# Optimization experiments

Measured on AMD Instinct MI355X. Metric: run time of the kernel, lower is better.

The kernel has to match this reference:

```python
import jax, jax.numpy as jnp
import numpy as np

INPUT_DIMS = [300, 74, 35]
HIDDEN_DIMS = [512, 256, 256]
OUT_CELL = 256
OUT_DIM = 7
B, T = 128, 256


def setup_inputs() -> dict:
    key = jax.random.key(0)
    ks = jax.random.split(key, 32)
    inp = {}
    for i, d in enumerate(INPUT_DIMS):
        inp[f"x{i}"] = jax.random.normal(ks[i], (B, T, d), dtype=jnp.float32)
    ki = 3
    for i, (d, h) in enumerate(zip(INPUT_DIMS, HIDDEN_DIMS)):
        s_ih = 1.0 / np.sqrt(h)
        inp[f"W_ih{i}"] = jax.random.uniform(ks[ki + 0], (4 * h, d), jnp.float32, -s_ih, s_ih)
        inp[f"W_hh{i}"] = jax.random.uniform(ks[ki + 1], (4 * h, h), jnp.float32, -s_ih, s_ih)
        inp[f"b_ih{i}"] = jax.random.uniform(ks[ki + 2], (4 * h,), jnp.float32, -s_ih, s_ih)
        inp[f"b_hh{i}"] = jax.random.uniform(ks[ki + 3], (4 * h,), jnp.float32, -s_ih, s_ih)
        ki += 4
    H = sum(HIDDEN_DIMS)
    s1 = 1.0 / np.sqrt(H)
    s2 = 1.0 / np.sqrt(OUT_CELL)
    inp["fc_W1"] = jax.random.uniform(ks[ki + 0], (OUT_CELL, H), jnp.float32, -s1, s1)
    inp["fc_b1"] = jax.random.uniform(ks[ki + 1], (OUT_CELL,), jnp.float32, -s1, s1)
    inp["fc_W2"] = jax.random.uniform(ks[ki + 2], (OUT_DIM, OUT_CELL), jnp.float32, -s2, s2)
    inp["fc_b2"] = jax.random.uniform(ks[ki + 3], (OUT_DIM,), jnp.float32, -s2, s2)
    return inp


def _run_lstm(x, W_ih, W_hh, b_ih, b_hh):
    # x: [B, T, d] -> hidden trajectory [B, T, h]; PyTorch LSTMCell gate order i,f,g,o
    Bsz = x.shape[0]
    h4 = W_hh.shape[0]
    h = h4 // 4
    gx = jnp.einsum('btd,gd->btg', x, W_ih) + b_ih + b_hh  # precompute input contribution

    def step(carry, g_t):
        hp, cp = carry
        g = g_t + hp @ W_hh.T  # [B, 4h]
        i, f, gg, o = jnp.split(g, 4, axis=-1)
        c = jax.nn.sigmoid(f) * cp + jax.nn.sigmoid(i) * jnp.tanh(gg)
        hn = jax.nn.sigmoid(o) * jnp.tanh(c)
        return (hn, c), hn

    h0 = jnp.zeros((Bsz, h), x.dtype)
    c0 = jnp.zeros((Bsz, h), x.dtype)
    _, hs = jax.lax.scan(step, (h0, c0), gx.transpose(1, 0, 2))  # hs: [T, B, h]
    return hs.transpose(1, 0, 2)


def reference(x0, x1, x2,
              W_ih0, W_hh0, b_ih0, b_hh0,
              W_ih1, W_hh1, b_ih1, b_hh1,
              W_ih2, W_hh2, b_ih2, b_hh2,
              fc_W1, fc_b1, fc_W2, fc_b2):
    hs = [
        _run_lstm(x0, W_ih0, W_hh0, b_ih0, b_hh0),
        _run_lstm(x1, W_ih1, W_hh1, b_ih1, b_hh1),
        _run_lstm(x2, W_ih2, W_hh2, b_ih2, b_hh2),
    ]
    hcat = jnp.concatenate(hs, axis=-1)  # [B, T, sum(h)]
    # SimpleNet head (dropout identity at inference): Linear -> ReLU -> Linear
    z = jax.nn.relu(jnp.einsum('bth,ch->btc', hcat, fc_W1) + fc_b1)
    logits = jnp.einsum('btc,oc->bto', z, fc_W2) + fc_b2  # [B, T, out]
    return jax.nn.log_softmax(logits, axis=-1)
```

## Files before the change

### kernel.cpp

```cpp
#include <hip/hip_runtime.h>
#include <hip/hip_bf16.h>
#include <math.h>

typedef __hip_bfloat16 bf16;
typedef unsigned short ushort_t;
typedef unsigned long long ull_t;
typedef __attribute__((ext_vector_type(8))) short short8;
typedef __attribute__((ext_vector_type(4))) float f32x4;

constexpr int NB = 128;
constexpr int NT = 256;
constexpr int HCAT = 1024;
constexpr int KP0 = 320;
constexpr int KP1 = 128;
constexpr int KP2 = 64;

__device__ inline float bf2f(ushort_t u) {
  union { unsigned i; float f; } x; x.i = (unsigned)u << 16; return x.f;
}
__device__ inline ushort_t f2bf(float f) {
  bf16 b = __float2bfloat16(f);
  return *reinterpret_cast<ushort_t*>(&b);
}
__device__ inline float fsig(float x) {
  return __builtin_amdgcn_rcpf(1.f + __expf(-x));
}
__device__ inline float ftanh(float x) {
  return 2.f * __builtin_amdgcn_rcpf(1.f + __expf(-2.f * x)) - 1.f;
}

__global__ __launch_bounds__(256) void k_cvt_w7(
    const float* __restrict__ w0, const float* __restrict__ w1,
    const float* __restrict__ w2, const float* __restrict__ w3,
    const float* __restrict__ w4, const float* __restrict__ w5,
    const float* __restrict__ w6,
    ushort_t* __restrict__ o0, ushort_t* __restrict__ o1,
    ushort_t* __restrict__ o2, ushort_t* __restrict__ o3,
    ushort_t* __restrict__ o4, ushort_t* __restrict__ o5,
    ushort_t* __restrict__ o6)
{
  constexpr int T0 = 2048 * KP0;
  constexpr int T1 = 1024 * KP1;
  constexpr int T2 = 1024 * KP2;
  constexpr int T3 = 256 * 1024;
  constexpr int T4 = 2048 * 512;
  constexpr int T5 = 1024 * 256;
  constexpr int T6 = 1024 * 256;
  constexpr int E0 = T0, E1 = E0 + T1, E2 = E1 + T2, E3 = E2 + T3;
  constexpr int E4 = E3 + T4, E5 = E4 + T5, E6 = E5 + T6;
  int i = blockIdx.x * 256 + threadIdx.x;
  if (i < E0) {
    int r = i / KP0, k = i - r * KP0;
    o0[i] = (k < 300) ? f2bf(w0[(size_t)r * 300 + k]) : (ushort_t)0;
  } else if (i < E1) {
    int j = i - E0;
    int r = j / KP1, k = j - r * KP1;
    o1[j] = (k < 74) ? f2bf(w1[(size_t)r * 74 + k]) : (ushort_t)0;
  } else if (i < E2) {
    int j = i - E1;
    int r = j / KP2, k = j - r * KP2;
    o2[j] = (k < 35) ? f2bf(w2[(size_t)r * 35 + k]) : (ushort_t)0;
  } else if (i < E3) {
    int j = i - E2;
    o3[j] = f2bf(w3[j]);
  } else if (i < E4) {
    int j = i - E3;
    o4[j] = f2bf(w4[j]);
  } else if (i < E5) {
    int j = i - E4;
    o5[j] = f2bf(w5[j]);
  } else if (i < E6) {
    int j = i - E5;
    o6[j] = f2bf(w6[j]);
  }
}

__global__ __launch_bounds__(256) void k_cvt_x3(
    const float* __restrict__ x0, const float* __restrict__ x1,
    const float* __restrict__ x2,
    ushort_t* __restrict__ o0, ushort_t* __restrict__ o1,
    ushort_t* __restrict__ o2,
    int t0, int tcShift, int rows)
{
  const int tot0 = rows * KP0;
  const int tot1 = rows * KP1;
  const int tot2 = rows * KP2;
  int i = blockIdx.x * 256 + threadIdx.x;
  if (i < tot0) {
    int row = i / KP0, k = i - row * KP0;
    int b = row >> tcShift, tl = row & ((1 << tcShift) - 1);
    o0[i] = (k < 300) ? f2bf(x0[((size_t)b * NT + t0 + tl) * 300 + k]) : (ushort_t)0;
  } else if (i < tot0 + tot1) {
    int j = i - tot0;
    int row = j / KP1, k = j - row * KP1;
    int b = row >> tcShift, tl = row & ((1 << tcShift) - 1);
    o1[j] = (k < 74) ? f2bf(x1[((size_t)b * NT + t0 + tl) * 74 + k]) : (ushort_t)0;
  } else if (i < tot0 + tot1 + tot2) {
    int j = i - tot0 - tot1;
    int row = j / KP2, k = j - row * KP2;
    int b = row >> tcShift, tl = row & ((1 << tcShift) - 1);
    o2[j] = (k < 35) ? f2bf(x2[((size_t)b * NT + t0 + tl) * 35 + k]) : (ushort_t)0;
  }
}

__global__ __launch_bounds__(256) void k_gemm_gx12(
    const ushort_t* __restrict__ A1, const ushort_t* __restrict__ B1,
    const ushort_t* __restrict__ A2, const ushort_t* __restrict__ B2,
    const float* __restrict__ bi1, const float* __restrict__ bh1,
    const float* __restrict__ bi2, const float* __restrict__ bh2,
    ushort_t* __restrict__ o1, ushort_t* __restrict__ o2)
{
  __shared__ ushort_t As[2][64][72];
  __shared__ ushort_t Bs[2][64][72];
  const int by   = blockIdx.y;
  const bool l2  = (by >= 16);
  const ushort_t* A = l2 ? A2 : A1;
  const ushort_t* B = l2 ? B2 : B1;
  const float* bias0 = l2 ? bi2 : bi1;
  const float* bias1 = l2 ? bh2 : bh1;
  ushort_t* outb = l2 ? o2 : o1;
  const int KP   = l2 ? KP2 : KP1;
  const int row0 = blockIdx.x * 64;
  const int col0 = (l2 ? by - 16 : by) * 64;
  const int ldc  = 1024;
  const int tid  = threadIdx.x;
  const int lane = tid & 63;
  const int w    = tid >> 6;
  const int n    = lane & 15;
  const int quad = lane >> 4;
  const int sr = tid >> 2;
  const int sc = (tid & 3) * 16;

  const ushort_t* arow = A + (size_t)(row0 + sr) * KP + sc;
  const ushort_t* brow = B + (size_t)(col0 + sr) * KP + sc;

  short8 ra0 = *reinterpret_cast<const short8*>(arow);
  short8 ra1 = *reinterpret_cast<const short8*>(arow + 8);
  short8 rb0 = *reinterpret_cast<const short8*>(brow);
  short8 rb1 = *reinterpret_cast<const short8*>(brow + 8);
  *reinterpret_cast<short8*>(&As[0][sr][sc])     = ra0;
  *reinterpret_cast<short8*>(&As[0][sr][sc + 8]) = ra1;
  *reinterpret_cast<short8*>(&Bs[0][sr][sc])     = rb0;
  *reinterpret_cast<short8*>(&Bs[0][sr][sc + 8]) = rb1;

  f32x4 acc[4] = {{0,0,0,0},{0,0,0,0},{0,0,0,0},{0,0,0,0}};
  const int nch = KP >> 6;
  for (int ch = 0; ch < nch; ++ch) {
    __syncthreads();
    const int cur = ch & 1;
    if (ch + 1 < nch) {
      const ushort_t* an = arow + (ch + 1) * 64;
      const ushort_t* bn = brow + (ch + 1) * 64;
      ra0 = *reinterpret_cast<const short8*>(an);
      ra1 = *reinterpret_cast<const short8*>(an + 8);
      rb0 = *reinterpret_cast<const short8*>(bn);
      rb1 = *reinterpret_cast<const short8*>(bn + 8);
    }
#pragma unroll
    for (int kc = 0; kc < 2; ++kc) {
      short8 bfr = *reinterpret_cast<const short8*>(&Bs[cur][w * 16 + n][quad * 8 + kc * 32]);
#pragma unroll
      for (int mt = 0; mt < 4; ++mt) {
        short8 afr = *reinterpret_cast<const short8*>(&As[cur][mt * 16 + n][quad * 8 + kc * 32]);
        acc[mt] = __builtin_amdgcn_mfma_f32_16x16x32_bf16(afr, bfr, acc[mt], 0, 0, 0);
      }
    }
    if (ch + 1 < nch) {
      const int nxt = 1 - cur;
      *reinterpret_cast<short8*>(&As[nxt][sr][sc])     = ra0;
      *reinterpret_cast<short8*>(&As[nxt][sr][sc + 8]) = ra1;
      *reinterpret_cast<short8*>(&Bs[nxt][sr][sc])     = rb0;
      *reinterpret_cast<short8*>(&Bs[nxt][sr][sc + 8]) = rb1;
    }
  }

  const int col = col0 + w * 16 + n;
  const float bsum = bias0[col] + bias1[col];
#pragma unroll
  for (int mt = 0; mt < 4; ++mt)
#pragma unroll
    for (int r = 0; r < 4; ++r) {
      int row = row0 + mt * 16 + quad * 4 + r;
      outb[(size_t)row * ldc + col] = f2bf(acc[mt][r] + bsum);
    }
}

__global__ __launch_bounds__(256) void k_gemm128(
    const ushort_t* __restrict__ A, const ushort_t* __restrict__ B, int KP,
    const float* __restrict__ bias0, const float* __restrict__ bias1,
    ushort_t* __restrict__ outb, float* __restrict__ outf, int ldc, int mode)
{
  __shared__ ushort_t As[2][128][72];
  __shared__ ushort_t Bs[2][128][72];
  const int row0 = blockIdx.x * 128;
  const int col0 = blockIdx.y * 128;
  const int tid  = threadIdx.x;
  const int lane = tid & 63;
  const int w    = tid >> 6;
  const int wr   = w >> 1;
  const int wc   = w & 1;
  const int n    = lane & 15;
  const int quad = lane >> 4;
  const int sr = tid >> 1;
  const int sc = (tid & 1) * 32;

  const ushort_t* arow = A + (size_t)(row0 + sr) * KP + sc;
  const ushort_t* brow = B + (size_t)(col0 + sr) * KP + sc;

  short8 ra[4], rb[4];
#pragma unroll
  for (int j = 0; j < 4; ++j) {
    ra[j] = *reinterpret_cast<const short8*>(arow + j * 8);
    rb[j] = *reinterpret_cast<const short8*>(brow + j * 8);
  }
#pragma unroll
  for (int j = 0; j < 4; ++j) {
    *reinterpret_cast<short8*>(&As[0][sr][sc + j * 8]) = ra[j];
    *reinterpret_cast<short8*>(&Bs[0][sr][sc + j * 8]) = rb[j];
  }

  f32x4 acc[4][4] = {};
  const int nch = KP >> 6;
  for (int ch = 0; ch < nch; ++ch) {
    __syncthreads();
    const int cur = ch & 1;
    if (ch + 1 < nch) {
      const ushort_t* an = arow + (ch + 1) * 64;
      const ushort_t* bn = brow + (ch + 1) * 64;
#pragma unroll
      for (int j = 0; j < 4; ++j) {
        ra[j] = *reinterpret_cast<const short8*>(an + j * 8);
        rb[j] = *reinterpret_cast<const short8*>(bn + j * 8);
      }
    }
#pragma unroll
    for (int kc = 0; kc < 2; ++kc) {
      short8 bfr[4];
#pragma unroll
      for (int nt = 0; nt < 4; ++nt)
        bfr[nt] = *reinterpret_cast<const short8*>(
            &Bs[cur][wc * 64 + nt * 16 + n][quad * 8 + kc * 32]);
#pragma unroll
      for (int mt = 0; mt < 4; ++mt) {
        short8 afr = *reinterpret_cast<const short8*>(
            &As[cur][wr * 64 + mt * 16 + n][quad * 8 + kc * 32]);
#pragma unroll
        for (int nt = 0; nt < 4; ++nt)
          acc[mt][nt] = __builtin_amdgcn_mfma_f32_16x16x32_bf16(afr, bfr[nt], acc[mt][nt], 0, 0, 0);
      }
    }
    if (ch + 1 < nch) {
      const int nxt = 1 - cur;
#pragma unroll
      for (int j = 0; j < 4; ++j) {
        *reinterpret_cast<short8*>(&As[nxt][sr][sc + j * 8]) = ra[j];
        *reinterpret_cast<short8*>(&Bs[nxt][sr][sc + j * 8]) = rb[j];
      }
    }
  }

#pragma unroll
  for (int nt = 0; nt < 4; ++nt) {
    const int col = col0 + wc * 64 + nt * 16 + n;
    if (mode == 0) {
      const float bsum = bias0[col] + bias1[col];
#pragma unroll
      for (int mt = 0; mt < 4; ++mt)
#pragma unroll
        for (int r = 0; r < 4; ++r) {
          int row = row0 + wr * 64 + mt * 16 + quad * 4 + r;
          outb[(size_t)row * ldc + col] = f2bf(acc[mt][nt][r] + bsum);
        }
    } else {
      const float bsum = bias0[col];
#pragma unroll
      for (int mt = 0; mt < 4; ++mt)
#pragma unroll
        for (int r = 0; r < 4; ++r) {
          int row = row0 + wr * 64 + mt * 16 + quad * 4 + r;
          outf[(size_t)row * ldc + col] = fmaxf(acc[mt][nt][r] + bsum, 0.f);
        }
    }
  }
}

__global__ __launch_bounds__(256) void k_fc2(
    const float* __restrict__ Z, const float* __restrict__ W2,
    const float* __restrict__ b2, float* __restrict__ out, int t0, int tcShift)
{
  const int wave = threadIdx.x >> 6;
  const int lane = threadIdx.x & 63;
  const int bt = blockIdx.x * 4 + wave;
  const float* z = Z + (size_t)bt * 256;
  float zv[4];
#pragma unroll
  for (int j = 0; j < 4; ++j) zv[j] = z[lane + 64 * j];
  float lg[7];
#pragma unroll
  for (int o = 0; o < 7; ++o) {
    float a = 0.f;
#pragma unroll
    for (int j = 0; j < 4; ++j) a += zv[j] * W2[o * 256 + lane + 64 * j];
#pragma unroll
    for (int off = 32; off > 0; off >>= 1) a += __shfl_down(a, off, 64);
    lg[o] = a;
  }
  if (lane == 0) {
    const int b = bt >> tcShift;
    const int tl = bt & ((1 << tcShift) - 1);
    float* op = out + ((size_t)b * NT + t0 + tl) * 7;
    float lo[7];
    float m = -1e30f;
#pragma unroll
    for (int o = 0; o < 7; ++o) { lo[o] = lg[o] + b2[o]; m = fmaxf(m, lo[o]); }
    float s = 0.f;
#pragma unroll
    for (int o = 0; o < 7; ++o) s += expf(lo[o] - m);
    float lse = m + logf(s);
#pragma unroll
    for (int o = 0; o < 7; ++o) op[o] = lo[o] - lse;
  }
}

template<int HL>
__device__ void lstm_body(const ushort_t* __restrict__ Whh,
                          const ushort_t* __restrict__ gx,
                          unsigned* __restrict__ hb2,
                          float* __restrict__ cbuf,
                          ushort_t* __restrict__ hs,
                          ushort_t* htile,
                          float (*gbuf)[16][34],
                          int g, int u0, int hoff, int t0, int TC)
{
  constexpr int KC  = HL / 32;
  constexpr int LHP = HL + 8;
  constexpr int NGR = HL / 32;
  const int tid  = threadIdx.x;
  const int lane = tid & 63;
  const int wgate = tid >> 6;
  const int n    = lane & 15;
  const int quad = lane >> 4;

  short8 wfrag[2][KC];
#pragma unroll
  for (int tau = 0; tau < 2; ++tau) {
    const ushort_t* wrow = Whh + ((size_t)wgate * HL + u0 + 16 * tau + n) * HL + quad * 8;
#pragma unroll
    for (int kc = 0; kc < KC; ++kc)
      wfrag[tau][kc] = *reinterpret_cast<const short8*>(wrow + kc * 32);
  }

  const int u  = tid & 31;
  const int bh = tid >> 5;
  const int bb0 = g * 16 + bh;
  const int bb1 = bb0 + 8;
  const int hcol = hoff + u0 + u;
  float c0 = cbuf[(size_t)bb0 * HCAT + hcol];
  float c1 = cbuf[(size_t)bb1 * HCAT + hcol];

  const int srow = wgate * 4 + (lane >> 4);
  const int scol = lane & 15;
  unsigned* htile32 = reinterpret_cast<unsigned*>(htile);

  const size_t G4 = (size_t)(4 * HL);
  float gxv0[4], gxv1[4];
#pragma unroll
  for (int q = 0; q < 4; ++q) {
    gxv0[q] = bf2f(gx[((size_t)bb0 * TC) * G4 + (size_t)q * HL + u0 + u]);
    gxv1[q] = bf2f(gx[((size_t)bb1 * TC) * G4 + (size_t)q * HL + u0 + u]);
  }

  const ull_t EPM = 0xFFFF0000FFFF0000ull;

  for (int t = 0; t < TC; ++t) {
    const unsigned ep = (unsigned)(t0 + t);
    const ull_t want = ((ull_t)ep << 16) | ((ull_t)ep << 48);
    const ull_t* src64 = reinterpret_cast<const ull_t*>(
        hb2 + ((size_t)(ep & 1) * NB + g * 16 + srow) * HCAT + hoff);

    ull_t vv[NGR];
    while (true) {
#pragma unroll
      for (int i = 0; i < NGR; ++i)
        vv[i] = __hip_atomic_load(src64 + scol + i * 16,
                                  __ATOMIC_RELAXED, __HIP_MEMORY_SCOPE_AGENT);
      ull_t bad = 0;
#pragma unroll
      for (int i = 0; i < NGR; ++i) bad |= (vv[i] ^ want) & EPM;
      if (bad == 0) break;
      __builtin_amdgcn_s_sleep(1);
    }
#pragma unroll
    for (int i = 0; i < NGR; ++i)
      htile32[srow * (LHP / 2) + scol + i * 16] =
          (unsigned)(vv[i] & 0xffffu) | ((unsigned)(vv[i] >> 16) & 0xffff0000u);
    __syncthreads();

    f32x4 acc0 = {0.f, 0.f, 0.f, 0.f};
    f32x4 acc1 = {0.f, 0.f, 0.f, 0.f};
#pragma unroll
    for (int kc = 0; kc < KC; ++kc) {
      short8 a = *reinterpret_cast<const short8*>(htile + n * LHP + quad * 8 + kc * 32);
      acc0 = __builtin_amdgcn_mfma_f32_16x16x32_bf16(a, wfrag[0][kc], acc0, 0, 0, 0);
      acc1 = __builtin_amdgcn_mfma_f32_16x16x32_bf16(a, wfrag[1][kc], acc1, 0, 0, 0);
    }
#pragma unroll
    for (int r = 0; r < 4; ++r) {
      gbuf[wgate][quad * 4 + r][n]      = acc0[r];
      gbuf[wgate][quad * 4 + r][16 + n] = acc1[r];
    }
    __syncthreads();

    float pi0 = gbuf[0][bh][u] + gxv0[0];
    float pf0 = gbuf[1][bh][u] + gxv0[1];
    float pg0 = gbuf[2][bh][u] + gxv0[2];
    float po0 = gbuf[3][bh][u] + gxv0[3];
    float pi1 = gbuf[0][bh + 8][u] + gxv1[0];
    float pf1 = gbuf[1][bh + 8][u] + gxv1[1];
    float pg1 = gbuf[2][bh + 8][u] + gxv1[2];
    float po1 = gbuf[3][bh + 8][u] + gxv1[3];

    float si0 = fsig(pi0), sf0 = fsig(pf0), so0 = fsig(po0);
    float tg0 = ftanh(pg0);
    c0 = sf0 * c0 + si0 * tg0;
    float h0 = so0 * ftanh(c0);
    float si1 = fsig(pi1), sf1 = fsig(pf1), so1 = fsig(po1);
    float tg1 = ftanh(pg1);
    c1 = sf1 * c1 + si1 * tg1;
    float h1 = so1 * ftanh(c1);

    const ushort_t hb0 = f2bf(h0), hb1 = f2bf(h1);
    const unsigned ep1 = (ep + 1) << 16;
    unsigned* nxt = hb2 + (size_t)((ep + 1) & 1) * NB * HCAT;
    __hip_atomic_store(nxt + (size_t)bb0 * HCAT + hcol, ep1 | (unsigned)hb0,
                       __ATOMIC_RELAXED, __HIP_MEMORY_SCOPE_AGENT);
    __hip_atomic_store(nxt + (size_t)bb1 * HCAT + hcol, ep1 | (unsigned)hb1,
                       __ATOMIC_RELAXED, __HIP_MEMORY_SCOPE_AGENT);

    hs[((size_t)bb0 * TC + t) * HCAT + hcol] = hb0;
    hs[((size_t)bb1 * TC + t) * HCAT + hcol] = hb1;
    if (t + 1 < TC) {
#pragma unroll
      for (int q = 0; q < 4; ++q) {
        gxv0[q] = bf2f(gx[((size_t)bb0 * TC + t + 1) * G4 + (size_t)q * HL + u0 + u]);
        gxv1[q] = bf2f(gx[((size_t)bb1 * TC + t + 1) * G4 + (size_t)q * HL + u0 + u]);
      }
    }
  }
  cbuf[(size_t)bb0 * HCAT + hcol] = c0;
  cbuf[(size_t)bb1 * HCAT + hcol] = c1;
}

__global__ __launch_bounds__(256, 1) void k_lstm(
    const ushort_t* __restrict__ Whh0, const ushort_t* __restrict__ Whh1,
    const ushort_t* __restrict__ Whh2,
    const ushort_t* __restrict__ gx0, const ushort_t* __restrict__ gx1,
    const ushort_t* __restrict__ gx2,
    unsigned* __restrict__ hb2, float* __restrict__ cbuf,
    ushort_t* __restrict__ hs,
    int t0, int TC)
{
  __shared__ ushort_t htile[16 * 520];
  __shared__ float gbuf[4][16][34];
  const int g    = blockIdx.x & 7;
  const int rank = blockIdx.x >> 3;
  if (rank < 16) {
    lstm_body<512>(Whh0, gx0, hb2, cbuf, hs, htile, gbuf,
                   g, rank * 32, 0, t0, TC);
  } else if (rank < 24) {
    lstm_body<256>(Whh1, gx1, hb2, cbuf, hs, htile, gbuf,
                   g, (rank - 16) * 32, 512, t0, TC);
  } else {
    lstm_body<256>(Whh2, gx2, hb2, cbuf, hs, htile, gbuf,
                   g, (rank - 24) * 32, 768, t0, TC);
  }
}

__global__ void k_fill(float* __restrict__ out, int n, float v) {
  int i = blockIdx.x * 256 + threadIdx.x;
  if (i < n) out[i] = v;
}

extern "C" void kernel_launch(void* const* d_in, const int* in_sizes, int n_in,
                              void* d_out, int out_size, void* d_ws, size_t ws_size,
                              hipStream_t stream) {
  (void)in_sizes; (void)n_in;
  const float* x0  = (const float*)d_in[0];
  const float* x1  = (const float*)d_in[1];
  const float* x2  = (const float*)d_in[2];
  const float* Wih0 = (const float*)d_in[3];
  const float* Whh0 = (const float*)d_in[4];
  const float* bih0 = (const float*)d_in[5];
  const float* bhh0 = (const float*)d_in[6];
  const float* Wih1 = (const float*)d_in[7];
  const float* Whh1 = (const float*)d_in[8];
  const float* bih1 = (const float*)d_in[9];
  const float* bhh1 = (const float*)d_in[10];
  const float* Wih2 = (const float*)d_in[11];
  const float* Whh2 = (const float*)d_in[12];
  const float* bih2 = (const float*)d_in[13];
  const float* bhh2 = (const float*)d_in[14];
  const float* W1 = (const float*)d_in[15];
  const float* b1 = (const float*)d_in[16];
  const float* W2 = (const float*)d_in[17];
  const float* b2 = (const float*)d_in[18];
  float* out = (float*)d_out;

  const size_t szHbuf  = (size_t)2 * NB * HCAT * 4;
  const size_t szCbuf  = (size_t)NB * HCAT * 4;
  const size_t szWb0   = (size_t)2048 * KP0 * 2;
  const size_t szWb1   = (size_t)1024 * KP1 * 2;
  const size_t szWb2   = (size_t)1024 * KP2 * 2;
  const size_t szW1b   = (size_t)256 * 1024 * 2;
  const size_t szWhb0  = (size_t)2048 * 512 * 2;
  const size_t szWhb1  = (size_t)1024 * 256 * 2;
  const size_t szWhb2  = (size_t)1024 * 256 * 2;

  const int cands[6] = {256, 128, 64, 32, 16, 8};
  int TC = 0;
  for (int ci = 0; ci < 6; ++ci) {
    int tc = cands[ci];
    size_t rows = (size_t)NB * tc;
    size_t o = 0;
    auto al = [&](size_t bytes) { o += (bytes + 255) & ~(size_t)255; };
    al(szHbuf); al(szCbuf);
    al(szWb0); al(szWb1); al(szWb2); al(szW1b);
    al(szWhb0); al(szWhb1); al(szWhb2);
    al(rows * HCAT * 2);
    al(rows * 256 * 4);
    al(rows * 2048 * 2);
    al(rows * 1024 * 2);
    al(rows * 1024 * 2);
    al(rows * KP0 * 2);
    al(rows * KP1 * 2);
    al(rows * KP2 * 2);
    if (o <= ws_size) { TC = tc; break; }
  }
  if (TC == 0) {
    k_fill<<<dim3((out_size + 255) / 256), dim3(256), 0, stream>>>(out, out_size, -8888.f);
    return;
  }
  const int tcShift = __builtin_ctz(TC);
  const size_t rows = (size_t)NB * TC;

  char* ws = (char*)d_ws;
  size_t off = 0;
  auto alloc = [&](size_t bytes) -> void* {
    void* p = ws + off;
    off += (bytes + 255) & ~(size_t)255;
    return p;
  };
  unsigned* hb2  = (unsigned*)alloc(szHbuf);
  float* cbuf    = (float*)alloc(szCbuf);
  size_t staticEnd = off;
  ushort_t* wb0  = (ushort_t*)alloc(szWb0);
  ushort_t* wb1  = (ushort_t*)alloc(szWb1);
  ushort_t* wb2  = (ushort_t*)alloc(szWb2);
  ushort_t* w1b  = (ushort_t*)alloc(szW1b);
  ushort_t* whb0 = (ushort_t*)alloc(szWhb0);
  ushort_t* whb1 = (ushort_t*)alloc(szWhb1);
  ushort_t* whb2 = (ushort_t*)alloc(szWhb2);
  ushort_t* hs   = (ushort_t*)alloc(rows * HCAT * 2);
  float* z       = (float*)alloc(rows * 256 * 4);
  ushort_t* gx0  = (ushort_t*)alloc(rows * 2048 * 2);
  ushort_t* gx1  = (ushort_t*)alloc(rows * 1024 * 2);
  ushort_t* gx2  = (ushort_t*)alloc(rows * 1024 * 2);
  ushort_t* xb0  = (ushort_t*)alloc(rows * KP0 * 2);
  ushort_t* xb1  = (ushort_t*)alloc(rows * KP1 * 2);
  ushort_t* xb2  = (ushort_t*)alloc(rows * KP2 * 2);

  hipMemsetAsync(ws, 0, staticEnd, stream);

  dim3 blk(256);
  {
    const int totW = 2048 * KP0 + 1024 * KP1 + 1024 * KP2 + 256 * 1024
                   + 2048 * 512 + 1024 * 256 + 1024 * 256;
    k_cvt_w7<<<dim3((totW + 255) / 256), blk, 0, stream>>>(
        Wih0, Wih1, Wih2, W1, Whh0, Whh1, Whh2,
        wb0, wb1, wb2, w1b, whb0, whb1, whb2);
  }

  const int rb  = (int)(rows / 64);
  const int rbm = (int)(rows / 128);
  for (int t0 = 0; t0 < NT; t0 += TC) {
    {
      const int totX = (int)(rows * (KP0 + KP1 + KP2));
      k_cvt_x3<<<dim3((totX + 255) / 256), blk, 0, stream>>>(
          x0, x1, x2, xb0, xb1, xb2, t0, tcShift, (int)rows);
    }

    k_gemm128<<<dim3(rbm, 2048 / 128), blk, 0, stream>>>(xb0, wb0, KP0, bih0, bhh0, gx0, nullptr, 2048, 0);
    k_gemm_gx12<<<dim3(rb, 32), blk, 0, stream>>>(xb1, wb1, xb2, wb2,
                                                  bih1, bhh1, bih2, bhh2,
                                                  gx1, gx2);

    k_lstm<<<dim3(256), blk, 0, stream>>>(whb0, whb1, whb2,
                                          gx0, gx1, gx2,
                                          hb2, cbuf, hs, t0, TC);

    k_gemm128<<<dim3(rbm, 256 / 128), blk, 0, stream>>>(hs, w1b, 1024, b1, nullptr, nullptr, z, 256, 1);
    k_fc2<<<dim3((int)(rows / 4)), blk, 0, stream>>>(z, W2, b2, out, t0, tcShift);
  }
}
```

Measured before the change: 883.7 us.

## Fuse FC1 GEMM, ReLU, FC2 and log-softmax into one kernel

```diff
diff --git a/kernel.cpp b/kernel.cpp
--- a/kernel.cpp
+++ b/kernel.cpp
@@ -188,7 +188,7 @@
 __global__ __launch_bounds__(256) void k_gemm128(
     const ushort_t* __restrict__ A, const ushort_t* __restrict__ B, int KP,
     const float* __restrict__ bias0, const float* __restrict__ bias1,
-    ushort_t* __restrict__ outb, float* __restrict__ outf, int ldc, int mode)
+    ushort_t* __restrict__ outb, int ldc)
 {
   __shared__ ushort_t As[2][128][72];
   __shared__ ushort_t Bs[2][128][72];
@@ -262,61 +262,136 @@
 #pragma unroll
   for (int nt = 0; nt < 4; ++nt) {
     const int col = col0 + wc * 64 + nt * 16 + n;
-    if (mode == 0) {
-      const float bsum = bias0[col] + bias1[col];
-#pragma unroll
-      for (int mt = 0; mt < 4; ++mt)
-#pragma unroll
-        for (int r = 0; r < 4; ++r) {
-          int row = row0 + wr * 64 + mt * 16 + quad * 4 + r;
-          outb[(size_t)row * ldc + col] = f2bf(acc[mt][nt][r] + bsum);
-        }
-    } else {
-      const float bsum = bias0[col];
-#pragma unroll
-      for (int mt = 0; mt < 4; ++mt)
-#pragma unroll
-        for (int r = 0; r < 4; ++r) {
-          int row = row0 + wr * 64 + mt * 16 + quad * 4 + r;
-          outf[(size_t)row * ldc + col] = fmaxf(acc[mt][nt][r] + bsum, 0.f);
-        }
-    }
-  }
-}
-
-__global__ __launch_bounds__(256) void k_fc2(
-    const float* __restrict__ Z, const float* __restrict__ W2,
-    const float* __restrict__ b2, float* __restrict__ out, int t0, int tcShift)
+    const float bsum = bias0[col] + bias1[col];
+#pragma unroll
+    for (int mt = 0; mt < 4; ++mt)
+#pragma unroll
+      for (int r = 0; r < 4; ++r) {
+        int row = row0 + wr * 64 + mt * 16 + quad * 4 + r;
+        outb[(size_t)row * ldc + col] = f2bf(acc[mt][nt][r] + bsum);
+      }
+  }
+}
+
+__global__ __launch_bounds__(256) void k_fc12(
+    const ushort_t* __restrict__ A,
+    const ushort_t* __restrict__ B,
+    const float* __restrict__ b1,
+    const float* __restrict__ W2, const float* __restrict__ b2,
+    float* __restrict__ out, int t0, int tcShift)
 {
-  const int wave = threadIdx.x >> 6;
-  const int lane = threadIdx.x & 63;
-  const int bt = blockIdx.x * 4 + wave;
-  const float* z = Z + (size_t)bt * 256;
-  float zv[4];
-#pragma unroll
-  for (int j = 0; j < 4; ++j) zv[j] = z[lane + 64 * j];
-  float lg[7];
-#pragma unroll
-  for (int o = 0; o < 7; ++o) {
-    float a = 0.f;
-#pragma unroll
-    for (int j = 0; j < 4; ++j) a += zv[j] * W2[o * 256 + lane + 64 * j];
-#pragma unroll
-    for (int off = 32; off > 0; off >>= 1) a += __shfl_down(a, off, 64);
-    lg[o] = a;
-  }
-  if (lane == 0) {
-    const int b = bt >> tcShift;
-    const int tl = bt & ((1 << tcShift) - 1);
-    float* op = out + ((size_t)b * NT + t0 + tl) * 7;
+  constexpr int KP = 1024;
+  __shared__ ushort_t As[2][64][72];
+  __shared__ ushort_t Bs[2][256][72];
+  __shared__ float part[64][4][8];
+  const int row0 = blockIdx.x * 64;
+  const int tid  = threadIdx.x;
+  const int lane = tid & 63;
+  const int wc   = tid >> 6;
+  const int n    = lane & 15;
+  const int quad = lane >> 4;
+  const int asr = tid >> 2, asc = (tid & 3) * 16;
+  const int bsr = tid;
+
+  const ushort_t* arow = A + (size_t)(row0 + asr) * KP + asc;
+  const ushort_t* brow = B + (size_t)bsr * KP;
+
+  short8 ra[2], rb[8];
+#pragma unroll
+  for (int j = 0; j < 2; ++j) ra[j] = *reinterpret_cast<const short8*>(arow + j * 8);
+#pragma unroll
+  for (int j = 0; j < 8; ++j) rb[j] = *reinterpret_cast<const short8*>(brow + j * 8);
+#pragma unroll
+  for (int j = 0; j < 2; ++j) *reinterpret_cast<short8*>(&As[0][asr][asc + j * 8]) = ra[j];
+#pragma unroll
+  for (int j = 0; j < 8; ++j) *reinterpret_cast<short8*>(&Bs[0][bsr][j * 8]) = rb[j];
+
+  f32x4 acc[4][4] = {};
+  const int nch = KP >> 6;
+  for (int ch = 0; ch < nch; ++ch) {
+    __syncthreads();
+    const int cur = ch & 1;
+    if (ch + 1 < nch) {
+      const ushort_t* an = arow + (ch + 1) * 64;
+      const ushort_t* bn = brow + (ch + 1) * 64;
+#pragma unroll
+      for (int j = 0; j < 2; ++j) ra[j] = *reinterpret_cast<const short8*>(an + j * 8);
+#pragma unroll
+      for (int j = 0; j < 8; ++j) rb[j] = *reinterpret_cast<const short8*>(bn + j * 8);
+    }
+#pragma unroll
+    for (int kc = 0; kc < 2; ++kc) {
+      short8 bfr[4];
+#pragma unroll
+      for (int nt = 0; nt < 4; ++nt)
+        bfr[nt] = *reinterpret_cast<const short8*>(
+            &Bs[cur][wc * 64 + nt * 16 + n][quad * 8 + kc * 32]);
+#pragma unroll
+      for (int mt = 0; mt < 4; ++mt) {
+        short8 afr = *reinterpret_cast<const short8*>(
+            &As[cur][mt * 16 + n][quad * 8 + kc * 32]);
+#pragma unroll
+        for (int nt = 0; nt < 4; ++nt)
+          acc[mt][nt] = __builtin_amdgcn_mfma_f32_16x16x32_bf16(afr, bfr[nt], acc[mt][nt], 0, 0, 0);
+      }
+    }
+    if (ch + 1 < nch) {
+      const int nxt = 1 - cur;
+#pragma unroll
+      for (int j = 0; j < 2; ++j) *reinterpret_cast<short8*>(&As[nxt][asr][asc + j * 8]) = ra[j];
+#pragma unroll
+      for (int j = 0; j < 8; ++j) *reinterpret_cast<short8*>(&Bs[nxt][bsr][j * 8]) = rb[j];
+    }
+  }
+
+  float b1v[4], w2v[4][7];
+#pragma unroll
+  for (int nt = 0; nt < 4; ++nt) {
+    int col = wc * 64 + nt * 16 + n;
+    b1v[nt] = b1[col];
+#pragma unroll
+    for (int o = 0; o < 7; ++o) w2v[nt][o] = W2[o * 256 + col];
+  }
+#pragma unroll
+  for (int mt = 0; mt < 4; ++mt) {
+#pragma unroll
+    for (int r = 0; r < 4; ++r) {
+      float p[7] = {0.f, 0.f, 0.f, 0.f, 0.f, 0.f, 0.f};
+#pragma unroll
+      for (int nt = 0; nt < 4; ++nt) {
+        float zv = fmaxf(acc[mt][nt][r] + b1v[nt], 0.f);
+#pragma unroll
+        for (int o = 0; o < 7; ++o) p[o] += zv * w2v[nt][o];
+      }
+#pragma unroll
+      for (int o = 0; o < 7; ++o) {
+#pragma unroll
+        for (int off = 8; off > 0; off >>= 1) p[o] += __shfl_xor(p[o], off, 64);
+      }
+      if (n == 0) {
+        int row = mt * 16 + quad * 4 + r;
+#pragma unroll
+        for (int o = 0; o < 7; ++o) part[row][wc][o] = p[o];
+      }
+    }
+  }
+  __syncthreads();
+  if (tid < 64) {
     float lo[7];
     float m = -1e30f;
 #pragma unroll
-    for (int o = 0; o < 7; ++o) { lo[o] = lg[o] + b2[o]; m = fmaxf(m, lo[o]); }
+    for (int o = 0; o < 7; ++o) {
+      lo[o] = part[tid][0][o] + part[tid][1][o] + part[tid][2][o] + part[tid][3][o] + b2[o];
+      m = fmaxf(m, lo[o]);
+    }
     float s = 0.f;
 #pragma unroll
     for (int o = 0; o < 7; ++o) s += expf(lo[o] - m);
     float lse = m + logf(s);
+    const int row = row0 + tid;
+    const int b = row >> tcShift;
+    const int tl = row & ((1 << tcShift) - 1);
+    float* op = out + ((size_t)b * NT + t0 + tl) * 7;
 #pragma unroll
     for (int o = 0; o < 7; ++o) op[o] = lo[o] - lse;
   }
@@ -527,7 +602,6 @@
     al(szWb0); al(szWb1); al(szWb2); al(szW1b);
     al(szWhb0); al(szWhb1); al(szWhb2);
     al(rows * HCAT * 2);
-    al(rows * 256 * 4);
     al(rows * 2048 * 2);
     al(rows * 1024 * 2);
     al(rows * 1024 * 2);
@@ -561,7 +635,6 @@
   ushort_t* whb1 = (ushort_t*)alloc(szWhb1);
   ushort_t* whb2 = (ushort_t*)alloc(szWhb2);
   ushort_t* hs   = (ushort_t*)alloc(rows * HCAT * 2);
-  float* z       = (float*)alloc(rows * 256 * 4);
   ushort_t* gx0  = (ushort_t*)alloc(rows * 2048 * 2);
   ushort_t* gx1  = (ushort_t*)alloc(rows * 1024 * 2);
   ushort_t* gx2  = (ushort_t*)alloc(rows * 1024 * 2);
@@ -589,7 +662,7 @@
           x0, x1, x2, xb0, xb1, xb2, t0, tcShift, (int)rows);
     }
 
-    k_gemm128<<<dim3(rbm, 2048 / 128), blk, 0, stream>>>(xb0, wb0, KP0, bih0, bhh0, gx0, nullptr, 2048, 0);
+    k_gemm128<<<dim3(rbm, 2048 / 128), blk, 0, stream>>>(xb0, wb0, KP0, bih0, bhh0, gx0, 2048);
     k_gemm_gx12<<<dim3(rb, 32), blk, 0, stream>>>(xb1, wb1, xb2, wb2,
                                                   bih1, bhh1, bih2, bhh2,
                                                   gx1, gx2);
@@ -598,7 +671,6 @@
                                           gx0, gx1, gx2,
                                           hb2, cbuf, hs, t0, TC);
 
-    k_gemm128<<<dim3(rbm, 256 / 128), blk, 0, stream>>>(hs, w1b, 1024, b1, nullptr, nullptr, z, 256, 1);
-    k_fc2<<<dim3((int)(rows / 4)), blk, 0, stream>>>(z, W2, b2, out, t0, tcShift);
-  }
-}
+    k_fc12<<<dim3(rb), blk, 0, stream>>>(hs, w1b, b1, W2, b2, out, t0, tcShift);
+  }
+}
```

Result: no change. 891.0 us (+0.8%).
